# Kernel optimization log

Measured on AMD Instinct MI355X. Metric: run time of the kernel, lower is better.

The kernel has to match this reference:

```python
import jax, jax.numpy as jnp
import numpy as np


def setup_inputs() -> dict:
    key = jax.random.key(0)
    ks = jax.random.split(key, 8)
    B, L, C = 8, 4096, 1024
    H = C // 2
    return {
        "x": jax.random.normal(ks[0], (B, L, C), dtype=jnp.float32),
        "w1": jax.random.normal(ks[1], (C, 1), dtype=jnp.float32) * 0.02,
        "b1": jnp.zeros((1,), dtype=jnp.float32),
        "w2": jax.random.normal(ks[2], (C, H), dtype=jnp.float32) * 0.02,
        "b2": jnp.zeros((H,), dtype=jnp.float32),
        "w3": jax.random.normal(ks[3], (H, C), dtype=jnp.float32) * 0.02,
        "b3": jnp.zeros((C,), dtype=jnp.float32),
        "w4": jax.random.normal(ks[4], (C, H), dtype=jnp.float32) * 0.02,
        "b4": jnp.zeros((H,), dtype=jnp.float32),
        "w5": jax.random.normal(ks[5], (C, H), dtype=jnp.float32) * 0.02,
        "b5": jnp.zeros((H,), dtype=jnp.float32),
    }


def reference(x, w1, b1, w2, b2, w3, b3, w4, b4, w5, b5):
    # Polarized self-attention (keras): channel branch then spatial branch.
    B, L, C = x.shape
    # --- channel branch ---
    t1 = x @ w1 + b1                                   # conv1: [B, L, 1]
    t2 = x @ w2 + b2                                   # conv2: [B, L, C/2]
    a = jax.nn.softmax(t1.reshape(B, 1, L), axis=-1)   # reshape1 + softmax: [B, 1, L]
    t2 = jnp.einsum('bol,blh->boh', a, t2)             # dot1 (axes 2,1): [B, 1, C/2]
    t2 = jax.nn.sigmoid(t2 @ w3 + b3)                  # conv3 + sigmoid: [B, 1, C]
    # attention1([inputs, t2]): dot scores [B, L, 1]; softmax over key axis of
    # size 1 is exactly 1.0, so output is t2 broadcast across L (exact math).
    o = jnp.broadcast_to(t2, (B, L, C))                # [B, L, C]
    # --- spatial branch ---
    t1 = o @ w4 + b4                                   # conv4: [B, L, C/2]
    t2 = o @ w5 + b5                                   # conv5: [B, L, C/2]
    t1 = jnp.max(t1, axis=1)[:, :, None]               # global max pool + reshape2: [B, C/2, 1]
    s = jax.nn.sigmoid(jnp.einsum('bho,blh->bol', t1, t2))  # dot2 (axes 1,2) + sigmoid: [B, 1, L]
    # attention2([reshape(o, [B,C,L]), s]): scores [B, C, 1]; softmax over the
    # size-1 key axis is 1.0, so output is s broadcast to [B, C, L] (exact).
    out = jnp.broadcast_to(s, (B, C, L)).reshape(B, L, C)  # reshape4
    return out
```

## Files before the change

kernel.cpp:

```cpp
#include <hip/hip_runtime.h>
#include <stdint.h>

#define B 8
#define L 4096
#define C 1024
#define H 512
#define NPART 512
#define CCH 16

__global__ __launch_bounds__(256) void kA_fused(const float* __restrict__ x,
                                                const float* __restrict__ w1,
                                                const float* __restrict__ b1,
                                                float* __restrict__ partial_xa,
                                                float* __restrict__ partial_s,
                                                float* __restrict__ zero_targets) {
    __shared__ float4 lds[4][256];
    __shared__ float ldsS[4];
    int t = threadIdx.x;
    int wave = t >> 6, lane = t & 63;
    int b = blockIdx.x >> 6;
    int blkInB = blockIdx.x & 63;
    int l0 = blkInB * 64 + wave * 16;
    float b1v = b1[0];

    if (blockIdx.x < 48) zero_targets[blockIdx.x * 256 + t] = 0.f;

    const float4* w1v = (const float4*)w1;
    float4 wf[4];
#pragma unroll
    for (int k = 0; k < 4; ++k) wf[k] = w1v[lane + 64 * k];

    float4 acc[4];
#pragma unroll
    for (int k = 0; k < 4; ++k) acc[k] = make_float4(0.f, 0.f, 0.f, 0.f);
    float sexp = 0.f;

    for (int r = 0; r < 16; ++r) {
        const float4* row = (const float4*)(x + ((size_t)(b * L + l0 + r)) * C);
        float4 xv[4];
#pragma unroll
        for (int k = 0; k < 4; ++k) xv[k] = row[lane + 64 * k];
        float d = 0.f;
#pragma unroll
        for (int k = 0; k < 4; ++k)
            d += xv[k].x * wf[k].x + xv[k].y * wf[k].y + xv[k].z * wf[k].z + xv[k].w * wf[k].w;
#pragma unroll
        for (int off = 32; off > 0; off >>= 1) d += __shfl_xor(d, off, 64);
        float e = __expf(d + b1v);
        sexp += e;
#pragma unroll
        for (int k = 0; k < 4; ++k) {
            acc[k].x += e * xv[k].x;
            acc[k].y += e * xv[k].y;
            acc[k].z += e * xv[k].z;
            acc[k].w += e * xv[k].w;
        }
    }
#pragma unroll
    for (int k = 0; k < 4; ++k) lds[wave][lane + 64 * k] = acc[k];
    if (lane == 0) ldsS[wave] = sexp;
    __syncthreads();
    float4 s0 = lds[0][t], s1 = lds[1][t], s2 = lds[2][t], s3 = lds[3][t];
    float4 s4;
    s4.x = (s0.x + s1.x) + (s2.x + s3.x);
    s4.y = (s0.y + s1.y) + (s2.y + s3.y);
    s4.z = (s0.z + s1.z) + (s2.z + s3.z);
    s4.w = (s0.w + s1.w) + (s2.w + s3.w);
    ((float4*)partial_xa)[(size_t)blockIdx.x * 256 + t] = s4;
    if (t == 0) partial_s[blockIdx.x] = (ldsS[0] + ldsS[1]) + (ldsS[2] + ldsS[3]);
}

__global__ __launch_bounds__(256) void k4a_pooled(const float* __restrict__ partial_xa,
                                                  const float* __restrict__ partial_s,
                                                  const float* __restrict__ w2,
                                                  const float* __restrict__ b2,
                                                  float* __restrict__ pooled) {
    __shared__ float ldsS[512];
    __shared__ float invS[B];
    __shared__ float xs[B][CCH];
    int hg = blockIdx.x & 1;
    int cc = blockIdx.x >> 1;
    int c0 = cc * CCH;
    int t = threadIdx.x;

    ldsS[t] = partial_s[t];
    ldsS[t + 256] = partial_s[t + 256];
    __syncthreads();
    if (t < B) {
        float s = 0.f;
        for (int i = 0; i < 64; ++i) s += ldsS[t * 64 + i];
        invS[t] = 1.f / s;
    }
    __syncthreads();

    if (t < B * CCH) {
        int bb = t >> 4, ci = t & 15;
        float s = 0.f;
        const float* src = partial_xa + (size_t)(bb * 64) * C + c0 + ci;
        for (int j = 0; j < 64; ++j) s += src[(size_t)j * C];
        xs[bb][ci] = s * invS[bb];
    }
    __syncthreads();

    int h = hg * 256 + t;
    float acc[B] = {0.f, 0.f, 0.f, 0.f, 0.f, 0.f, 0.f, 0.f};
#pragma unroll
    for (int ci = 0; ci < CCH; ++ci) {
        float w = w2[(size_t)(c0 + ci) * H + h];
#pragma unroll
        for (int bb = 0; bb < B; ++bb) acc[bb] += xs[bb][ci] * w;
    }
    float bias = (cc == 0) ? b2[h] : 0.f;
#pragma unroll
    for (int bb = 0; bb < B; ++bb) atomicAdd(&pooled[bb * H + h], acc[bb] + bias);
}

__global__ __launch_bounds__(256) void k4bc(const float* __restrict__ pooled,
                                            const float* __restrict__ w3,
                                            const float* __restrict__ b3,
                                            const float* __restrict__ w4,
                                            const float* __restrict__ w5,
                                            float* __restrict__ u4raw,
                                            float* __restrict__ u5raw) {
    __shared__ float pooledS[B][H];
    __shared__ float vpart[16][B][CCH];
    __shared__ float vs[B][CCH];
    int hg = blockIdx.x & 1;
    int cc = blockIdx.x >> 1;
    int c0 = cc * CCH;
    int t = threadIdx.x;

    for (int i = t; i < B * H; i += 256) ((float*)pooledS)[i] = pooled[i];
    __syncthreads();

    {
        int ci = t & 15;
        int hq = t >> 4;
        float a[B] = {0.f, 0.f, 0.f, 0.f, 0.f, 0.f, 0.f, 0.f};
        for (int hh = 0; hh < 32; ++hh) {
            int h = hq * 32 + hh;
            float w = w3[(size_t)h * C + c0 + ci];
#pragma unroll
            for (int bb = 0; bb < B; ++bb) a[bb] += pooledS[bb][h] * w;
        }
#pragma unroll
        for (int bb = 0; bb < B; ++bb) vpart[hq][bb][ci] = a[bb];
    }
    __syncthreads();
    if (t < B * CCH) {
        int bb = t >> 4, ci = t & 15;
        float v = b3[c0 + ci];
#pragma unroll
        for (int q = 0; q < 16; ++q) v += vpart[q][bb][ci];
        vs[bb][ci] = 1.f / (1.f + __expf(-v));
    }
    __syncthreads();
    {
        int h = hg * 256 + t;
        float a4[B] = {0.f, 0.f, 0.f, 0.f, 0.f, 0.f, 0.f, 0.f};
        float a5[B] = {0.f, 0.f, 0.f, 0.f, 0.f, 0.f, 0.f, 0.f};
#pragma unroll
        for (int ci = 0; ci < CCH; ++ci) {
            float wa = w4[(size_t)(c0 + ci) * H + h];
            float wb = w5[(size_t)(c0 + ci) * H + h];
#pragma unroll
            for (int bb = 0; bb < B; ++bb) {
                a4[bb] += vs[bb][ci] * wa;
                a5[bb] += vs[bb][ci] * wb;
            }
        }
#pragma unroll
        for (int bb = 0; bb < B; ++bb) {
            atomicAdd(&u4raw[bb * H + h], a4[bb]);
            atomicAdd(&u5raw[bb * H + h], a5[bb]);
        }
    }
}

__global__ __launch_bounds__(256) void k5_fill(const float* __restrict__ u4raw, const float* __restrict__ b4,
                                               const float* __restrict__ u5raw, const float* __restrict__ b5,
                                               float* __restrict__ out) {
    __shared__ float red[256];
    int blk = blockIdx.x, t = threadIdx.x;
    int b = blk >> 8;
    int rg = blk & 255;
    float s = (u4raw[b * H + t] + b4[t]) * (u5raw[b * H + t] + b5[t])
            + (u4raw[b * H + 256 + t] + b4[256 + t]) * (u5raw[b * H + 256 + t] + b5[256 + t]);
    red[t] = s; __syncthreads();
    for (int st = 128; st > 0; st >>= 1) { if (t < st) red[t] += red[t + st]; __syncthreads(); }
    float sc = 1.f / (1.f + __expf(-red[0]));
    float4 s4 = make_float4(sc, sc, sc, sc);
    float4* o = (float4*)out + (size_t)b * (L * C / 4) + (size_t)rg * 4096;
#pragma unroll
    for (int k = 0; k < 16; ++k) o[t + 256 * k] = s4;
}

extern "C" void kernel_launch(void* const* d_in, const int* in_sizes, int n_in,
                              void* d_out, int out_size, void* d_ws, size_t ws_size,
                              hipStream_t stream) {
    const float* x  = (const float*)d_in[0];
    const float* w1 = (const float*)d_in[1];
    const float* b1 = (const float*)d_in[2];
    const float* w2 = (const float*)d_in[3];
    const float* b2 = (const float*)d_in[4];
    const float* w3 = (const float*)d_in[5];
    const float* b3 = (const float*)d_in[6];
    const float* w4 = (const float*)d_in[7];
    const float* b4 = (const float*)d_in[8];
    const float* w5 = (const float*)d_in[9];
    const float* b5 = (const float*)d_in[10];

    float* ws         = (float*)d_ws;
    float* partial_xa = ws;
    float* partial_s  = partial_xa + NPART * C;
    float* pooled     = partial_s + NPART;
    float* u4raw      = pooled + B * H;
    float* u5raw      = u4raw + B * H;

    kA_fused<<<NPART, 256, 0, stream>>>(x, w1, b1, partial_xa, partial_s, pooled);
    k4a_pooled<<<128, 256, 0, stream>>>(partial_xa, partial_s, w2, b2, pooled);
    k4bc<<<128, 256, 0, stream>>>(pooled, w3, b3, w4, w5, u4raw, u5raw);
    k5_fill<<<2048, 256, 0, stream>>>(u4raw, b4, u5raw, b5, (float*)d_out);
}
```

Baseline: 281.2 us.

## Split x-reduction across more blocks, preload rows, restructure pooled reduction, nontemporal fill

The first kernel now uses 2048 blocks of 4 rows per wave instead of 512 blocks of 16 rows, and issues all 16 row loads up front to raise memory-level parallelism. The second reduction kernel is rewritten per batch and channel chunk, so the larger partial buffer is summed in parallel with wave shuffles. The fill kernel swaps its LDS tree reduction for wave shuffles and writes output with nontemporal stores. The cost is four times as many partial sums written and reread (8 MB of workspace), which could offset the gain from better occupancy on the x stream.

Result: no change. 281.9 us (+0.3%).

```diff
diff --git a/kernel.cpp b/kernel.cpp
--- a/kernel.cpp
+++ b/kernel.cpp
@@ -5,8 +5,12 @@
 #define L 4096
 #define C 1024
 #define H 512
-#define NPART 512
+#define NPART 2048
+#define NPB 256
 #define CCH 16
+#define CC4A 32
+
+typedef float nfloat4 __attribute__((ext_vector_type(4)));
 
 __global__ __launch_bounds__(256) void kA_fused(const float* __restrict__ x,
                                                 const float* __restrict__ w1,
@@ -18,9 +22,9 @@
     __shared__ float ldsS[4];
     int t = threadIdx.x;
     int wave = t >> 6, lane = t & 63;
-    int b = blockIdx.x >> 6;
-    int blkInB = blockIdx.x & 63;
-    int l0 = blkInB * 64 + wave * 16;
+    int b = blockIdx.x >> 8;
+    int blkInB = blockIdx.x & 255;
+    int l0 = blkInB * 16 + wave * 4;
     float b1v = b1[0];
 
     if (blockIdx.x < 48) zero_targets[blockIdx.x * 256 + t] = 0.f;
@@ -30,30 +34,36 @@
 #pragma unroll
     for (int k = 0; k < 4; ++k) wf[k] = w1v[lane + 64 * k];
 
+    const float4* row0 = (const float4*)(x + ((size_t)(b * L + l0)) * C);
+    float4 xv[4][4];
+#pragma unroll
+    for (int r = 0; r < 4; ++r)
+#pragma unroll
+        for (int k = 0; k < 4; ++k)
+            xv[r][k] = row0[r * 256 + lane + 64 * k];
+
     float4 acc[4];
 #pragma unroll
     for (int k = 0; k < 4; ++k) acc[k] = make_float4(0.f, 0.f, 0.f, 0.f);
     float sexp = 0.f;
 
-    for (int r = 0; r < 16; ++r) {
-        const float4* row = (const float4*)(x + ((size_t)(b * L + l0 + r)) * C);
-        float4 xv[4];
-#pragma unroll
-        for (int k = 0; k < 4; ++k) xv[k] = row[lane + 64 * k];
+#pragma unroll
+    for (int r = 0; r < 4; ++r) {
         float d = 0.f;
 #pragma unroll
         for (int k = 0; k < 4; ++k)
-            d += xv[k].x * wf[k].x + xv[k].y * wf[k].y + xv[k].z * wf[k].z + xv[k].w * wf[k].w;
+            d += xv[r][k].x * wf[k].x + xv[r][k].y * wf[k].y
+               + xv[r][k].z * wf[k].z + xv[r][k].w * wf[k].w;
 #pragma unroll
         for (int off = 32; off > 0; off >>= 1) d += __shfl_xor(d, off, 64);
         float e = __expf(d + b1v);
         sexp += e;
 #pragma unroll
         for (int k = 0; k < 4; ++k) {
-            acc[k].x += e * xv[k].x;
-            acc[k].y += e * xv[k].y;
-            acc[k].z += e * xv[k].z;
-            acc[k].w += e * xv[k].w;
+            acc[k].x += e * xv[r][k].x;
+            acc[k].y += e * xv[r][k].y;
+            acc[k].z += e * xv[r][k].z;
+            acc[k].w += e * xv[r][k].w;
         }
     }
 #pragma unroll
@@ -75,44 +85,50 @@
                                                   const float* __restrict__ w2,
                                                   const float* __restrict__ b2,
                                                   float* __restrict__ pooled) {
-    __shared__ float ldsS[512];
-    __shared__ float invS[B];
-    __shared__ float xs[B][CCH];
-    int hg = blockIdx.x & 1;
-    int cc = blockIdx.x >> 1;
-    int c0 = cc * CCH;
+    __shared__ float red[8][CC4A];
+    __shared__ float xs[CC4A];
+    __shared__ float sred[4];
+    __shared__ float invS;
     int t = threadIdx.x;
-
-    ldsS[t] = partial_s[t];
-    ldsS[t + 256] = partial_s[t + 256];
-    __syncthreads();
-    if (t < B) {
-        float s = 0.f;
-        for (int i = 0; i < 64; ++i) s += ldsS[t * 64 + i];
-        invS[t] = 1.f / s;
-    }
-    __syncthreads();
-
-    if (t < B * CCH) {
-        int bb = t >> 4, ci = t & 15;
-        float s = 0.f;
-        const float* src = partial_xa + (size_t)(bb * 64) * C + c0 + ci;
-        for (int j = 0; j < 64; ++j) s += src[(size_t)j * C];
-        xs[bb][ci] = s * invS[bb];
-    }
-    __syncthreads();
-
-    int h = hg * 256 + t;
-    float acc[B] = {0.f, 0.f, 0.f, 0.f, 0.f, 0.f, 0.f, 0.f};
-#pragma unroll
-    for (int ci = 0; ci < CCH; ++ci) {
-        float w = w2[(size_t)(c0 + ci) * H + h];
-#pragma unroll
-        for (int bb = 0; bb < B; ++bb) acc[bb] += xs[bb][ci] * w;
-    }
-    float bias = (cc == 0) ? b2[h] : 0.f;
-#pragma unroll
-    for (int bb = 0; bb < B; ++bb) atomicAdd(&pooled[bb * H + h], acc[bb] + bias);
+    int b = blockIdx.x >> 5;
+    int cc = blockIdx.x & 31;
+    int c0 = cc * CC4A;
+    int wave = t >> 6, lane = t & 63;
+
+    float ps = partial_s[b * NPB + t];
+#pragma unroll
+    for (int off = 32; off > 0; off >>= 1) ps += __shfl_xor(ps, off, 64);
+    if (lane == 0) sred[wave] = ps;
+
+    {
+        int ci = t & 31, jg = t >> 5;
+        float a = 0.f;
+        const float* src = partial_xa + ((size_t)(b * NPB + jg * 32)) * C + c0 + ci;
+#pragma unroll 8
+        for (int i = 0; i < 32; ++i) a += src[(size_t)i * C];
+        __syncthreads();
+        if (t == 0) invS = 1.f / ((sred[0] + sred[1]) + (sred[2] + sred[3]));
+        red[jg][ci] = a;
+    }
+    __syncthreads();
+    if (t < CC4A) {
+        float a = 0.f;
+#pragma unroll
+        for (int q = 0; q < 8; ++q) a += red[q][t];
+        xs[t] = a * invS;
+    }
+    __syncthreads();
+
+    float a0 = 0.f, a1 = 0.f;
+#pragma unroll 8
+    for (int ci = 0; ci < CC4A; ++ci) {
+        float xc = xs[ci];
+        a0 += xc * w2[(size_t)(c0 + ci) * H + t];
+        a1 += xc * w2[(size_t)(c0 + ci) * H + 256 + t];
+    }
+    if (cc == 0) { a0 += b2[t]; a1 += b2[t + 256]; }
+    atomicAdd(&pooled[b * H + t], a0);
+    atomicAdd(&pooled[b * H + 256 + t], a1);
 }
 
 __global__ __launch_bounds__(256) void k4bc(const float* __restrict__ pooled,
@@ -180,19 +196,23 @@
 __global__ __launch_bounds__(256) void k5_fill(const float* __restrict__ u4raw, const float* __restrict__ b4,
                                                const float* __restrict__ u5raw, const float* __restrict__ b5,
                                                float* __restrict__ out) {
-    __shared__ float red[256];
+    __shared__ float r4[4];
     int blk = blockIdx.x, t = threadIdx.x;
     int b = blk >> 8;
     int rg = blk & 255;
     float s = (u4raw[b * H + t] + b4[t]) * (u5raw[b * H + t] + b5[t])
             + (u4raw[b * H + 256 + t] + b4[256 + t]) * (u5raw[b * H + 256 + t] + b5[256 + t]);
-    red[t] = s; __syncthreads();
-    for (int st = 128; st > 0; st >>= 1) { if (t < st) red[t] += red[t + st]; __syncthreads(); }
-    float sc = 1.f / (1.f + __expf(-red[0]));
-    float4 s4 = make_float4(sc, sc, sc, sc);
-    float4* o = (float4*)out + (size_t)b * (L * C / 4) + (size_t)rg * 4096;
-#pragma unroll
-    for (int k = 0; k < 16; ++k) o[t + 256 * k] = s4;
+#pragma unroll
+    for (int off = 32; off > 0; off >>= 1) s += __shfl_xor(s, off, 64);
+    if ((t & 63) == 0) r4[t >> 6] = s;
+    __syncthreads();
+    float tot = (r4[0] + r4[1]) + (r4[2] + r4[3]);
+    float sc = 1.f / (1.f + __expf(-tot));
+    nfloat4 s4 = {sc, sc, sc, sc};
+    nfloat4* o = (nfloat4*)out + (size_t)b * (L * C / 4) + (size_t)rg * 4096;
+#pragma unroll
+    for (int k = 0; k < 16; ++k)
+        __builtin_nontemporal_store(s4, &o[t + 256 * k]);
 }
 
 extern "C" void kernel_launch(void* const* d_in, const int* in_sizes, int n_in,
@@ -212,13 +232,13 @@
 
     float* ws         = (float*)d_ws;
     float* partial_xa = ws;
-    float* partial_s  = partial_xa + NPART * C;
+    float* partial_s  = partial_xa + (size_t)NPART * C;
     float* pooled     = partial_s + NPART;
     float* u4raw      = pooled + B * H;
     float* u5raw      = u4raw + B * H;
 
     kA_fused<<<NPART, 256, 0, stream>>>(x, w1, b1, partial_xa, partial_s, pooled);
-    k4a_pooled<<<128, 256, 0, stream>>>(partial_xa, partial_s, w2, b2, pooled);
+    k4a_pooled<<<256, 256, 0, stream>>>(partial_xa, partial_s, w2, b2, pooled);
     k4bc<<<128, 256, 0, stream>>>(pooled, w3, b3, w4, w5, u4raw, u5raw);
     k5_fill<<<2048, 256, 0, stream>>>(u4raw, b4, u5raw, b5, (float*)d_out);
 }
```
